# Kernel optimization log

Hardware: AMD Instinct MI355X
Metric: run time of the kernel (lower is better)

## Reference

```python
import jax, jax.numpy as jnp
import numpy as np

EPS = 1e-12  # torch F.normalize eps

def _l2n(x, axis):
    n = jnp.linalg.norm(x, axis=axis, keepdims=True)
    return x / jnp.maximum(n, EPS)

def setup_inputs() -> dict:
    key = jax.random.key(0)
    ks = jax.random.split(key, 11)
    B, N, D = 8, 4096, 512
    s = 1.0 / np.sqrt(D)
    return {
        'a': jax.random.normal(ks[0], (B, N, D), jnp.float32),
        'b': jax.random.normal(ks[1], (B, N, D), jnp.float32),
        'Wq': jax.random.normal(ks[2], (D, D), jnp.float32) * s,
        'bq': jax.random.normal(ks[3], (D,), jnp.float32) * s,
        'Wk': jax.random.normal(ks[4], (D, D), jnp.float32) * s,
        'bk': jax.random.normal(ks[5], (D,), jnp.float32) * s,
        'w_g': jax.random.normal(ks[6], (D, 1), jnp.float32),
        'Wp': jax.random.normal(ks[7], (D, D), jnp.float32) * s,
        'bp': jax.random.normal(ks[8], (D,), jnp.float32) * s,
        'Wf': jax.random.normal(ks[9], (D, D), jnp.float32) * s,
        'bf': jax.random.normal(ks[10], (D,), jnp.float32) * s,
    }

def reference(a, b, Wq, bq, Wk, bk, w_g, Wp, bp, Wf, bf):
    D = a.shape[-1]
    scale = D ** (-0.5)
    query = _l2n(jnp.einsum('bnd,ed->bne', a, Wq) + bq, axis=-1)   # [B,N,D]
    key = _l2n(jnp.einsum('bnd,ed->bne', b, Wk) + bk, axis=-1)     # [B,N,D]
    A = (query @ w_g) * scale                                      # [B,N,1]
    A = _l2n(A, axis=1)                                            # normalize over seq
    G = jnp.sum(A * query, axis=1)                                 # [B,D] learned pooling
    gk = G[:, None, :] * key                                       # broadcast [B,N,D]
    out = jnp.einsum('bnd,ed->bne', gk, Wp) + bp + query           # residual
    out = jnp.einsum('bnd,ed->bne', out, Wf) + bf
    return out
```

## Files before the change

kernel.cpp:

```cpp
#include <hip/hip_runtime.h>
#include <stdint.h>

#define DD 512
#define MTOT 32768

typedef float f32x4 __attribute__((ext_vector_type(4)));
typedef __bf16 bf16x8 __attribute__((ext_vector_type(8)));

static __device__ __forceinline__ unsigned short f2bf(float f) {
  union { float f; unsigned int u; } c; c.f = f;
  unsigned int r = c.u + 0x7fffu + ((c.u >> 16) & 1u);
  return (unsigned short)(r >> 16);
}
static __device__ __forceinline__ float bf2f(unsigned short h) {
  union { unsigned int u; float f; } c; c.u = ((unsigned int)h) << 16;
  return c.f;
}

union FragU { uint4 u; bf16x8 b; };

static __device__ __forceinline__ void load_lds16(const void* g, void* l) {
  __builtin_amdgcn_global_load_lds(
      (const __attribute__((address_space(1))) void*)g,
      (__attribute__((address_space(3))) void*)l, 16, 0, 0);
}

__global__ __launch_bounds__(256) void cvt_all_k(
    const float* __restrict__ a, const float* __restrict__ b,
    const float* __restrict__ W0, const float* __restrict__ W1,
    const float* __restrict__ W2,
    unsigned short* __restrict__ da, unsigned short* __restrict__ db,
    unsigned short* __restrict__ D0, unsigned short* __restrict__ D1,
    unsigned short* __restrict__ D2, float* __restrict__ stats) {
  const int gx = blockIdx.x, tid = threadIdx.x;
  if (gx < 768) {
    int slab = gx >> 8;
    int off = ((gx & 255) * 256 + tid) * 4;
    const float* s = slab == 0 ? W0 : slab == 1 ? W1 : W2;
    unsigned short* d = slab == 0 ? D0 : slab == 1 ? D1 : D2;
    float4 f = *(const float4*)(s + off);
    ushort4 h;
    h.x = f2bf(f.x); h.y = f2bf(f.y); h.z = f2bf(f.z); h.w = f2bf(f.w);
    *(ushort4*)(d + off) = h;
  } else if (gx < 868) {
    int i = ((gx - 768) * 256 + tid) * 4;
    *(float4*)(stats + i) = make_float4(0.f, 0.f, 0.f, 0.f);
  } else {
    const int u = gx - 868;
    const float* s = (u >> 10) ? b : a;
    unsigned short* d = (u >> 10) ? db : da;
    const size_t base = ((size_t)(u & 1023) * 256 + tid) * 8;
#pragma unroll
    for (int t = 0; t < 8; t++) {
      size_t i = base + (size_t)t * 2097152;
      f32x4 f0 = *(const f32x4*)(s + i);
      f32x4 f1 = *(const f32x4*)(s + i + 4);
      union { uint4 u4; unsigned short h[8]; } pk;
      pk.h[0] = f2bf(f0.x); pk.h[1] = f2bf(f0.y);
      pk.h[2] = f2bf(f0.z); pk.h[3] = f2bf(f0.w);
      pk.h[4] = f2bf(f1.x); pk.h[5] = f2bf(f1.y);
      pk.h[6] = f2bf(f1.z); pk.h[7] = f2bf(f1.w);
      *(uint4*)(d + i) = pk.u4;
    }
  }
}

__global__ __launch_bounds__(256) void scalew_k(const float* __restrict__ Wp,
    const float* __restrict__ G, unsigned short* __restrict__ out) {
  int i = (blockIdx.x * 256 + threadIdx.x) * 4;
  int b = i >> 18;
  int rem = i & 262143;
  int d = rem & 511;
  float4 w = *(const float4*)(Wp + rem);
  float4 g = *(const float4*)(G + b * DD + d);
  ushort4 h;
  h.x = f2bf(w.x * g.x); h.y = f2bf(w.y * g.y);
  h.z = f2bf(w.z * g.z); h.w = f2bf(w.w * g.w);
  *(ushort4*)(out + i) = h;
}

static __device__ __forceinline__ void gemm_core(
    const unsigned short* __restrict__ X, const unsigned short* __restrict__ W,
    int row0, int col0, unsigned short* As, unsigned short* Bs,
    f32x4 (&acc)[4][4]) {
  const int tid = threadIdx.x;
  const int lane = tid & 63, wave = tid >> 6;
  const int sr = lane >> 3;
  const int scol = ((lane & 7) ^ sr) * 8;
  const unsigned short* Ag = X + (size_t)(row0 + wave * 32 + sr) * DD + scol;
  const unsigned short* Bg = W + (size_t)(col0 + wave * 32 + sr) * DD + scol;
  const int ldsb = wave * 32 * 64;
  const int fr = lane & 15, quad = lane >> 4;
  const int wr = (wave >> 1) * 64, wc = (wave & 1) * 64;
  const int sw0 = ((quad ^ (fr & 7)) * 8);
  const int sw1 = (((quad + 4) ^ (fr & 7)) * 8);

  for (int k0 = 0; k0 < DD; k0 += 64) {
#pragma unroll
    for (int q = 0; q < 4; q++) {
      load_lds16(Ag + (size_t)q * 8 * DD + k0, As + ldsb + q * 8 * 64);
      load_lds16(Bg + (size_t)q * 8 * DD + k0, Bs + ldsb + q * 8 * 64);
    }
    __syncthreads();
#pragma unroll
    for (int kk = 0; kk < 2; kk++) {
      const int sw = kk ? sw1 : sw0;
      bf16x8 af[4], bfr[4];
#pragma unroll
      for (int i = 0; i < 4; i++) {
        FragU u; u.u = *(const uint4*)&As[(wr + i * 16 + fr) * 64 + sw];
        af[i] = u.b;
      }
#pragma unroll
      for (int j = 0; j < 4; j++) {
        FragU u; u.u = *(const uint4*)&Bs[(wc + j * 16 + fr) * 64 + sw];
        bfr[j] = u.b;
      }
#pragma unroll
      for (int i = 0; i < 4; i++)
#pragma unroll
        for (int j = 0; j < 4; j++)
          acc[i][j] = __builtin_amdgcn_mfma_f32_16x16x32_bf16(af[i], bfr[j], acc[i][j], 0, 0, 0);
    }
    __syncthreads();
  }
}

__global__ __launch_bounds__(256) void gemm_qk_k(
    const unsigned short* __restrict__ Xq, const unsigned short* __restrict__ Xk,
    const unsigned short* __restrict__ Wqw, const unsigned short* __restrict__ Wkw,
    const float* __restrict__ bq, const float* __restrict__ bk,
    const float* __restrict__ wg,
    float* __restrict__ ssqQ, float* __restrict__ ssqK, float* __restrict__ Pdot,
    unsigned short* __restrict__ Cq, unsigned short* __restrict__ Ck) {
  __shared__ unsigned short As[128 * 64];
  __shared__ unsigned short Bs[128 * 64];
  const int isK = blockIdx.x >> 8;
  const int row0 = (blockIdx.x & 255) * 128, col0 = blockIdx.y * 128;
  const unsigned short* X = isK ? Xk : Xq;
  const unsigned short* W = isK ? Wkw : Wqw;
  const float* bias = isK ? bk : bq;
  float* ssq = isK ? ssqK : ssqQ;
  unsigned short* C = isK ? Ck : Cq;

  f32x4 acc[4][4] = {};
  gemm_core(X, W, row0, col0, As, Bs, acc);

  const int lane = threadIdx.x & 63, wave = threadIdx.x >> 6;
  const int fr = lane & 15, quad = lane >> 4;
  const int wr = (wave >> 1) * 64, wc = (wave & 1) * 64;
  const int colbase = col0 + wc + fr;
  float bv4[4], wg4[4];
#pragma unroll
  for (int j = 0; j < 4; j++) bv4[j] = bias[colbase + j * 16];
  if (!isK) {
#pragma unroll
    for (int j = 0; j < 4; j++) wg4[j] = wg[colbase + j * 16];
  }
#pragma unroll
  for (int i = 0; i < 4; i++) {
#pragma unroll
    for (int r = 0; r < 4; r++) {
      const int row = row0 + wr + i * 16 + quad * 4 + r;
      float ssum = 0.f, dsum = 0.f;
#pragma unroll
      for (int j = 0; j < 4; j++) {
        size_t idx = (size_t)row * DD + colbase + j * 16;
        float v = acc[i][j][r] + bv4[j];
        C[idx] = f2bf(v);
        ssum += v * v;
        if (!isK) dsum += v * wg4[j];
      }
#pragma unroll
      for (int m = 1; m < 16; m <<= 1) ssum += __shfl_xor(ssum, m, 64);
      if (!isK) {
#pragma unroll
        for (int m = 1; m < 16; m <<= 1) dsum += __shfl_xor(dsum, m, 64);
      }
      if (fr == 0) {
        atomicAdd(&ssq[row], ssum);
        if (!isK) atomicAdd(&Pdot[row], dsum);
      }
    }
  }
}

template<int BBATCH, int EMODE>
__global__ __launch_bounds__(256) void gemm_k(
    const unsigned short* __restrict__ X,
    const unsigned short* __restrict__ Wb,
    const float* __restrict__ bias,
    const unsigned short* __restrict__ Qadd,
    const float* __restrict__ qinv,
    const float* __restrict__ kinv,
    void* __restrict__ Cv) {
  __shared__ unsigned short As[128 * 64];
  __shared__ unsigned short Bs[128 * 64];
  const int row0 = blockIdx.x * 128, col0 = blockIdx.y * 128;
  const unsigned short* W = Wb + (BBATCH ? (size_t)(row0 >> 12) * 262144 : 0);

  f32x4 acc[4][4] = {};
  gemm_core(X, W, row0, col0, As, Bs, acc);

  const int lane = threadIdx.x & 63, wave = threadIdx.x >> 6;
  const int fr = lane & 15, quad = lane >> 4;
  const int wr = (wave >> 1) * 64, wc = (wave & 1) * 64;
  const int colbase = col0 + wc + fr;
  float bv4[4];
#pragma unroll
  for (int j = 0; j < 4; j++) bv4[j] = bias[colbase + j * 16];
#pragma unroll
  for (int i = 0; i < 4; i++) {
#pragma unroll
    for (int r = 0; r < 4; r++) {
      const int row = row0 + wr + i * 16 + quad * 4 + r;
      float ki = 1.f, qi = 1.f;
      if (EMODE == 3) { ki = kinv[row]; qi = qinv[row]; }
#pragma unroll
      for (int j = 0; j < 4; j++) {
        size_t idx = (size_t)row * DD + colbase + j * 16;
        if (EMODE == 3) {
          float v = acc[i][j][r] * ki + bv4[j] + qi * bf2f(Qadd[idx]);
          ((unsigned short*)Cv)[idx] = f2bf(v);
        } else {
          ((float*)Cv)[idx] = acc[i][j][r] + bv4[j];
        }
      }
    }
  }
}

__global__ __launch_bounds__(256) void pool2_k(
    const float* __restrict__ ssqQ, const float* __restrict__ ssqK,
    const float* __restrict__ P, float* __restrict__ qinv,
    float* __restrict__ kinv, const unsigned short* __restrict__ Q,
    float* __restrict__ G) {
  const int b = blockIdx.x >> 5, chunk = blockIdx.x & 31;
  const int t = threadIdx.x, lane = t & 63, wave = t >> 6;
  __shared__ float sred[4];
  __shared__ float gred[4][512];

  float ss = 0.f;
  for (int i = t; i < 4096; i += 256) {
    int n = b * 4096 + i;
    float qi = 1.0f / fmaxf(sqrtf(ssqQ[n]), 1e-12f);
    float A = P[n] * qi;
    ss += A * A;
  }
#pragma unroll
  for (int m = 1; m < 64; m <<= 1) ss += __shfl_xor(ss, m, 64);
  if (lane == 0) sred[wave] = ss;
  if (t < 128) {
    int n = b * 4096 + chunk * 128 + t;
    qinv[n] = 1.0f / fmaxf(sqrtf(ssqQ[n]), 1e-12f);
    kinv[n] = 1.0f / fmaxf(sqrtf(ssqK[n]), 1e-12f);
  }
  __syncthreads();
  const float sinv_b =
      1.0f / fmaxf(sqrtf(sred[0] + sred[1] + sred[2] + sred[3]), 1e-12f);

  float acc[8] = {};
  const int r0 = b * 4096 + chunk * 128 + wave * 32;
  for (int r = 0; r < 32; r++) {
    const int n = r0 + r;
    float qi = 1.0f / fmaxf(sqrtf(ssqQ[n]), 1e-12f);
    float wrow = P[n] * qi * qi * sinv_b;
    uint4 u = *(const uint4*)(Q + (size_t)n * DD + lane * 8);
    const unsigned short* h = (const unsigned short*)&u;
#pragma unroll
    for (int j = 0; j < 8; j++) acc[j] += wrow * bf2f(h[j]);
  }
#pragma unroll
  for (int j = 0; j < 8; j++) gred[wave][lane * 8 + j] = acc[j];
  __syncthreads();
  float g0 = gred[0][t] + gred[1][t] + gred[2][t] + gred[3][t];
  float g1 = gred[0][t + 256] + gred[1][t + 256] + gred[2][t + 256] + gred[3][t + 256];
  atomicAdd(&G[b * DD + t], g0);
  atomicAdd(&G[b * DD + t + 256], g1);
}

extern "C" void kernel_launch(void* const* d_in, const int* in_sizes, int n_in,
                              void* d_out, int out_size, void* d_ws, size_t ws_size,
                              hipStream_t stream) {
  const float* a   = (const float*)d_in[0];
  const float* b   = (const float*)d_in[1];
  const float* Wq  = (const float*)d_in[2];
  const float* bq  = (const float*)d_in[3];
  const float* Wk  = (const float*)d_in[4];
  const float* bk  = (const float*)d_in[5];
  const float* wg  = (const float*)d_in[6];
  const float* Wp  = (const float*)d_in[7];
  const float* bp  = (const float*)d_in[8];
  const float* Wf  = (const float*)d_in[9];
  const float* bfb = (const float*)d_in[10];

  const size_t WELEM = 262144;
  const size_t MD = (size_t)MTOT * DD;

  unsigned short* B0 = (unsigned short*)d_ws;
  unsigned short* B1 = B0 + MD;
  unsigned short* B2 = B1 + MD;
  unsigned short* B3 = B2 + MD;
  unsigned short* Wqb = B3 + MD;
  unsigned short* Wkb = Wqb + WELEM;
  unsigned short* Wfb = Wkb + WELEM;
  unsigned short* Wps = Wfb + WELEM;
  float* stats = (float*)(Wps + 8 * WELEM);
  float* ssqQ  = stats;
  float* ssqK  = stats + MTOT;
  float* Pd    = stats + 2 * MTOT;
  float* G     = stats + 3 * MTOT;
  float* qinv  = G + 4096;
  float* kinv  = qinv + MTOT;

  cvt_all_k<<<dim3(2916), dim3(256), 0, stream>>>(
      a, b, Wq, Wk, Wf, B0, B1, Wqb, Wkb, Wfb, stats);
  gemm_qk_k<<<dim3(512, 4), dim3(256), 0, stream>>>(
      B0, B1, Wqb, Wkb, bq, bk, wg, ssqQ, ssqK, Pd, B2, B3);
  pool2_k<<<dim3(256), dim3(256), 0, stream>>>(ssqQ, ssqK, Pd, qinv, kinv, B2, G);
  scalew_k<<<dim3(2048), dim3(256), 0, stream>>>(Wp, G, Wps);
  gemm_k<1, 3><<<dim3(256, 4), dim3(256), 0, stream>>>(
      B3, Wps, bp, B2, qinv, kinv, B0);
  gemm_k<0, 4><<<dim3(256, 4), dim3(256), 0, stream>>>(
      B0, Wfb, bfb, nullptr, nullptr, nullptr, d_out);
}
```

Before: 325.8 us.

## Fuse fp32-to-bf16 input conversion into QK GEMM and swizzle block order

The separate pass that converts the a and b activations to bf16 is removed. The QK GEMM now loads fp32 tiles straight into LDS with an XOR swizzle and converts them to bf16 while building MFMA fragments, which saves writing and re-reading 2x32MB of bf16 intermediates. All GEMM grids are flattened to 1D with a block-index swizzle that changes which tiles run together, aiming for better L2 reuse. In exchange the QK GEMM moves twice as many bytes into LDS per tile and does the conversion work inside the inner loop.

```diff
diff --git a/kernel.cpp b/kernel.cpp
--- a/kernel.cpp
+++ b/kernel.cpp
@@ -25,44 +25,23 @@
       (__attribute__((address_space(3))) void*)l, 16, 0, 0);
 }
 
-__global__ __launch_bounds__(256) void cvt_all_k(
-    const float* __restrict__ a, const float* __restrict__ b,
-    const float* __restrict__ W0, const float* __restrict__ W1,
-    const float* __restrict__ W2,
-    unsigned short* __restrict__ da, unsigned short* __restrict__ db,
+__global__ __launch_bounds__(256) void cvt3w_k(const float* __restrict__ W0,
+    const float* __restrict__ W1, const float* __restrict__ W2,
     unsigned short* __restrict__ D0, unsigned short* __restrict__ D1,
     unsigned short* __restrict__ D2, float* __restrict__ stats) {
-  const int gx = blockIdx.x, tid = threadIdx.x;
-  if (gx < 768) {
-    int slab = gx >> 8;
-    int off = ((gx & 255) * 256 + tid) * 4;
-    const float* s = slab == 0 ? W0 : slab == 1 ? W1 : W2;
-    unsigned short* d = slab == 0 ? D0 : slab == 1 ? D1 : D2;
-    float4 f = *(const float4*)(s + off);
-    ushort4 h;
-    h.x = f2bf(f.x); h.y = f2bf(f.y); h.z = f2bf(f.z); h.w = f2bf(f.w);
-    *(ushort4*)(d + off) = h;
-  } else if (gx < 868) {
-    int i = ((gx - 768) * 256 + tid) * 4;
+  int slab = blockIdx.x >> 8;
+  if (slab == 3) {
+    int i = ((blockIdx.x - 768) * 256 + threadIdx.x) * 4;
     *(float4*)(stats + i) = make_float4(0.f, 0.f, 0.f, 0.f);
-  } else {
-    const int u = gx - 868;
-    const float* s = (u >> 10) ? b : a;
-    unsigned short* d = (u >> 10) ? db : da;
-    const size_t base = ((size_t)(u & 1023) * 256 + tid) * 8;
-#pragma unroll
-    for (int t = 0; t < 8; t++) {
-      size_t i = base + (size_t)t * 2097152;
-      f32x4 f0 = *(const f32x4*)(s + i);
-      f32x4 f1 = *(const f32x4*)(s + i + 4);
-      union { uint4 u4; unsigned short h[8]; } pk;
-      pk.h[0] = f2bf(f0.x); pk.h[1] = f2bf(f0.y);
-      pk.h[2] = f2bf(f0.z); pk.h[3] = f2bf(f0.w);
-      pk.h[4] = f2bf(f1.x); pk.h[5] = f2bf(f1.y);
-      pk.h[6] = f2bf(f1.z); pk.h[7] = f2bf(f1.w);
-      *(uint4*)(d + i) = pk.u4;
-    }
-  }
+    return;
+  }
+  int off = ((blockIdx.x & 255) * 256 + threadIdx.x) * 4;
+  const float* s = slab == 0 ? W0 : slab == 1 ? W1 : W2;
+  unsigned short* d = slab == 0 ? D0 : slab == 1 ? D1 : D2;
+  float4 f = *(const float4*)(s + off);
+  ushort4 h;
+  h.x = f2bf(f.x); h.y = f2bf(f.y); h.z = f2bf(f.z); h.w = f2bf(f.w);
+  *(ushort4*)(d + off) = h;
 }
 
 __global__ __launch_bounds__(256) void scalew_k(const float* __restrict__ Wp,
@@ -127,28 +106,88 @@
 }
 
 __global__ __launch_bounds__(256) void gemm_qk_k(
-    const unsigned short* __restrict__ Xq, const unsigned short* __restrict__ Xk,
+    const float* __restrict__ Xa, const float* __restrict__ Xb,
     const unsigned short* __restrict__ Wqw, const unsigned short* __restrict__ Wkw,
     const float* __restrict__ bq, const float* __restrict__ bk,
     const float* __restrict__ wg,
     float* __restrict__ ssqQ, float* __restrict__ ssqK, float* __restrict__ Pdot,
     unsigned short* __restrict__ Cq, unsigned short* __restrict__ Ck) {
-  __shared__ unsigned short As[128 * 64];
+  __shared__ float AsF[128 * 64];
   __shared__ unsigned short Bs[128 * 64];
-  const int isK = blockIdx.x >> 8;
-  const int row0 = (blockIdx.x & 255) * 128, col0 = blockIdx.y * 128;
-  const unsigned short* X = isK ? Xk : Xq;
+  const int swz = (blockIdx.x & 7) * 256 + (blockIdx.x >> 3);
+  const int isK = swz >> 10;
+  const int t = swz & 1023;
+  const int row0 = (t >> 2) * 128, col0 = (t & 3) * 128;
+  const float* X = isK ? Xb : Xa;
   const unsigned short* W = isK ? Wkw : Wqw;
   const float* bias = isK ? bk : bq;
   float* ssq = isK ? ssqK : ssqQ;
   unsigned short* C = isK ? Ck : Cq;
 
-  f32x4 acc[4][4] = {};
-  gemm_core(X, W, row0, col0, As, Bs, acc);
-
   const int lane = threadIdx.x & 63, wave = threadIdx.x >> 6;
+
+  const int rl = lane >> 4;
+  const int gsE = (lane & 15) ^ (rl << 1);
+  const int gsO = gsE ^ 1;
+  const float* AgE = X + (size_t)(row0 + wave * 32 + rl) * DD + gsE * 4;
+  const float* AgO = X + (size_t)(row0 + wave * 32 + rl) * DD + gsO * 4;
+  const int ldsA = wave * 2048;
+
+  const int sr = lane >> 3;
+  const int scol = ((lane & 7) ^ sr) * 8;
+  const unsigned short* Bg = W + (size_t)(col0 + wave * 32 + sr) * DD + scol;
+  const int ldsb = wave * 32 * 64;
+
   const int fr = lane & 15, quad = lane >> 4;
   const int wr = (wave >> 1) * 64, wc = (wave & 1) * 64;
+  const int xorv = ((fr & 7) >> 2) | ((fr & 3) << 1);
+  const int swB0 = ((quad ^ (fr & 7)) * 8);
+  const int swB1 = (((quad + 4) ^ (fr & 7)) * 8);
+
+  f32x4 acc[4][4] = {};
+
+  for (int k0 = 0; k0 < DD; k0 += 64) {
+#pragma unroll
+    for (int q = 0; q < 8; q++) {
+      const float* src = ((q & 1) ? AgO : AgE) + (size_t)q * 4 * DD + k0;
+      load_lds16(src, AsF + ldsA + q * 256);
+    }
+#pragma unroll
+    for (int q = 0; q < 4; q++)
+      load_lds16(Bg + (size_t)q * 8 * DD + k0, Bs + ldsb + q * 8 * 64);
+    __syncthreads();
+#pragma unroll
+    for (int kk = 0; kk < 2; kk++) {
+      const int glo = ((kk * 4 + quad) * 2) ^ xorv;
+      const int ghi = glo ^ 1;
+      const int swB = kk ? swB1 : swB0;
+      bf16x8 af[4], bfr[4];
+#pragma unroll
+      for (int i = 0; i < 4; i++) {
+        const float* ap = &AsF[(wr + i * 16 + fr) * 64];
+        f32x4 lo = *(const f32x4*)(ap + glo * 4);
+        f32x4 hi = *(const f32x4*)(ap + ghi * 4);
+        bf16x8 v;
+        v[0] = (__bf16)lo.x; v[1] = (__bf16)lo.y;
+        v[2] = (__bf16)lo.z; v[3] = (__bf16)lo.w;
+        v[4] = (__bf16)hi.x; v[5] = (__bf16)hi.y;
+        v[6] = (__bf16)hi.z; v[7] = (__bf16)hi.w;
+        af[i] = v;
+      }
+#pragma unroll
+      for (int j = 0; j < 4; j++) {
+        FragU u; u.u = *(const uint4*)&Bs[(wc + j * 16 + fr) * 64 + swB];
+        bfr[j] = u.b;
+      }
+#pragma unroll
+      for (int i = 0; i < 4; i++)
+#pragma unroll
+        for (int j = 0; j < 4; j++)
+          acc[i][j] = __builtin_amdgcn_mfma_f32_16x16x32_bf16(af[i], bfr[j], acc[i][j], 0, 0, 0);
+    }
+    __syncthreads();
+  }
+
   const int colbase = col0 + wc + fr;
   float bv4[4], wg4[4];
 #pragma unroll
@@ -196,7 +235,8 @@
     void* __restrict__ Cv) {
   __shared__ unsigned short As[128 * 64];
   __shared__ unsigned short Bs[128 * 64];
-  const int row0 = blockIdx.x * 128, col0 = blockIdx.y * 128;
+  const int swz = (blockIdx.x & 7) * 128 + (blockIdx.x >> 3);
+  const int row0 = (swz >> 2) * 128, col0 = (swz & 3) * 128;
   const unsigned short* W = Wb + (BBATCH ? (size_t)(row0 >> 12) * 262144 : 0);
 
   f32x4 acc[4][4] = {};
@@ -297,11 +337,10 @@
   const size_t WELEM = 262144;
   const size_t MD = (size_t)MTOT * DD;
 
-  unsigned short* B0 = (unsigned short*)d_ws;
-  unsigned short* B1 = B0 + MD;
-  unsigned short* B2 = B1 + MD;
-  unsigned short* B3 = B2 + MD;
-  unsigned short* Wqb = B3 + MD;
+  unsigned short* O1b = (unsigned short*)d_ws;
+  unsigned short* Qb  = O1b + MD;
+  unsigned short* Kb  = Qb + MD;
+  unsigned short* Wqb = Kb + MD;
   unsigned short* Wkb = Wqb + WELEM;
   unsigned short* Wfb = Wkb + WELEM;
   unsigned short* Wps = Wfb + WELEM;
@@ -313,14 +352,13 @@
   float* qinv  = G + 4096;
   float* kinv  = qinv + MTOT;
 
-  cvt_all_k<<<dim3(2916), dim3(256), 0, stream>>>(
-      a, b, Wq, Wk, Wf, B0, B1, Wqb, Wkb, Wfb, stats);
-  gemm_qk_k<<<dim3(512, 4), dim3(256), 0, stream>>>(
-      B0, B1, Wqb, Wkb, bq, bk, wg, ssqQ, ssqK, Pd, B2, B3);
-  pool2_k<<<dim3(256), dim3(256), 0, stream>>>(ssqQ, ssqK, Pd, qinv, kinv, B2, G);
+  cvt3w_k<<<dim3(868), dim3(256), 0, stream>>>(Wq, Wk, Wf, Wqb, Wkb, Wfb, stats);
+  gemm_qk_k<<<dim3(2048), dim3(256), 0, stream>>>(
+      a, b, Wqb, Wkb, bq, bk, wg, ssqQ, ssqK, Pd, Qb, Kb);
+  pool2_k<<<dim3(256), dim3(256), 0, stream>>>(ssqQ, ssqK, Pd, qinv, kinv, Qb, G);
   scalew_k<<<dim3(2048), dim3(256), 0, stream>>>(Wp, G, Wps);
-  gemm_k<1, 3><<<dim3(256, 4), dim3(256), 0, stream>>>(
-      B3, Wps, bp, B2, qinv, kinv, B0);
-  gemm_k<0, 4><<<dim3(256, 4), dim3(256), 0, stream>>>(
-      B0, Wfb, bfb, nullptr, nullptr, nullptr, d_out);
-}
+  gemm_k<1, 3><<<dim3(1024), dim3(256), 0, stream>>>(
+      Kb, Wps, bp, Qb, qinv, kinv, O1b);
+  gemm_k<0, 4><<<dim3(1024), dim3(256), 0, stream>>>(
+      O1b, Wfb, bfb, nullptr, nullptr, nullptr, d_out);
+}
```

New measurement: 308.0 us. 1.06x faster.
